# Performance work log

Measured on AMD Instinct MI355X. Metric: run time of the kernel, lower is better.

The kernel has to match this reference:

```python
import jax, jax.numpy as jnp
import numpy as np

EPS = 1e-6
NUM_HEADS = 16


def setup_inputs() -> dict:
    key = jax.random.key(0)
    ks = jax.random.split(key, 11)
    B, S, E = 2, 2048, 1024
    sc = 1.0 / np.sqrt(E)
    return {
        "x": jax.random.normal(ks[0], (B, S, E), dtype=jnp.float32),
        "Wq": jax.random.normal(ks[1], (E, E), dtype=jnp.float32) * sc,
        "bq": jax.random.normal(ks[2], (E,), dtype=jnp.float32) * 0.01,
        "Wk": jax.random.normal(ks[3], (E, E), dtype=jnp.float32) * sc,
        "bk": jax.random.normal(ks[4], (E,), dtype=jnp.float32) * 0.01,
        "Wv": jax.random.normal(ks[5], (E, E), dtype=jnp.float32) * sc,
        "bv": jax.random.normal(ks[6], (E,), dtype=jnp.float32) * 0.01,
        "Wp": jax.random.normal(ks[7], (E, E), dtype=jnp.float32) * sc,
        "bp": jax.random.normal(ks[8], (E,), dtype=jnp.float32) * 0.01,
        "gain": jax.random.uniform(ks[9], (E,), dtype=jnp.float32),
        "beta": jax.random.normal(ks[10], (E,), dtype=jnp.float32),
    }


def _layer_norm(x, gain, beta):
    # torch: (x - mean) / (std + eps) * gain + bias, std with Bessel correction
    mean = jnp.mean(x, axis=-1, keepdims=True)
    std = jnp.std(x, axis=-1, keepdims=True, ddof=1)
    return (x - mean) / (std + EPS) * gain + beta


def reference(x, Wq, bq, Wk, bk, Wv, bv, Wp, bp, gain, beta):
    B, S, E = x.shape
    H = NUM_HEADS
    D = E // H
    # QKV projections, split heads: [B,S,E] -> [B,H,S,D]
    def heads(y):
        return y.reshape(B, S, H, D).transpose(0, 2, 1, 3)
    q = heads(x @ Wq + bq)
    k = heads(x @ Wk + bk)
    v = heads(x @ Wv + bv)
    # scores [B,H,S,S], mask=None path (no causal mask applied in forward)
    scores = jnp.einsum("bhid,bhjd->bhij", q, k) / jnp.sqrt(jnp.float32(D))
    attn = jax.nn.softmax(scores, axis=-1)  # dropout is identity at eval
    y = jnp.einsum("bhij,bhjd->bhid", attn, v)
    y = y.transpose(0, 2, 1, 3).reshape(B, S, E)
    return _layer_norm(y @ Wp + bp, gain, beta)
```

## Files before the change

### kernel.cpp

```cpp
#include <hip/hip_runtime.h>
#include <hip/hip_bf16.h>
#include <math.h>

constexpr int Bc = 2;
constexpr int Sc = 2048;
constexpr int Ec = 1024;
constexpr int Hc = 16;
constexpr int Dc = 64;

typedef __attribute__((ext_vector_type(8))) short short8;
typedef __attribute__((ext_vector_type(4))) short short4v;
typedef __attribute__((ext_vector_type(4))) int int4v;
typedef __attribute__((ext_vector_type(4))) float f32x4;

__device__ inline unsigned short f2bf(float x) {
    __hip_bfloat16 h = __float2bfloat16(x);
    return *reinterpret_cast<unsigned short*>(&h);
}

__device__ inline f32x4 mfma16(short8 a, short8 b, f32x4 c) {
    return __builtin_amdgcn_mfma_f32_16x16x32_bf16(a, b, c, 0, 0, 0);
}

__device__ inline float exp2_fast(float x) {
    float r;
    asm("v_exp_f32 %0, %1" : "=v"(r) : "v"(x));
    return r;
}

__device__ inline int cvt_pk_bf16(float lo, float hi) {
    int r;
    asm("v_cvt_pk_bf16_f32 %0, %1, %2" : "=v"(r) : "v"(lo), "v"(hi));
    return r;
}

__device__ inline void gload_lds16(const unsigned short* gsrc, unsigned short* ldst) {
    __builtin_amdgcn_global_load_lds(
        (const __attribute__((address_space(1))) unsigned int*)(const void*)gsrc,
        (__attribute__((address_space(3))) unsigned int*)(void*)ldst,
        16, 0, 0);
}

__global__ __launch_bounds__(256) void prep_kernel(
    const float* __restrict__ X, unsigned short* __restrict__ Xb,
    const float* __restrict__ W0, const float* __restrict__ W1,
    const float* __restrict__ W2, const float* __restrict__ W3,
    unsigned short* __restrict__ T0, unsigned short* __restrict__ T1,
    unsigned short* __restrict__ T2, unsigned short* __restrict__ T3)
{
    __shared__ unsigned short Ls[64][72];
    const int bid = blockIdx.x, t = threadIdx.x;
    if (bid < 2048) {
        int i = bid * 256 + t;
        const float4* src = (const float4*)(X + (size_t)i * 8);
        float4 a = src[0], b = src[1];
        short8 o;
        o[0] = f2bf(a.x); o[1] = f2bf(a.y); o[2] = f2bf(a.z); o[3] = f2bf(a.w);
        o[4] = f2bf(b.x); o[5] = f2bf(b.y); o[6] = f2bf(b.z); o[7] = f2bf(b.w);
        *(short8*)(Xb + (size_t)i * 8) = o;
        return;
    }
    const int tt = bid - 2048;
    const float* W; unsigned short* T;
    switch (tt >> 8) {
        case 0: W = W0; T = T0; break;
        case 1: W = W1; T = T1; break;
        case 2: W = W2; T = T2; break;
        default: W = W3; T = T3; break;
    }
    const int rem = tt & 255;
    const int n0 = (rem & 15) * 64, k0 = (rem >> 4) * 64;
    {
        int k = t >> 2, nb = (t & 3) * 16;
        const float* src = W + (size_t)(k0 + k) * Ec + n0 + nb;
#pragma unroll
        for (int j = 0; j < 16; ++j) Ls[k][nb + j] = f2bf(src[j]);
    }
    __syncthreads();
    {
        int n = t >> 2, kb = (t & 3) * 16;
        short8 o0, o1;
#pragma unroll
        for (int j = 0; j < 8; ++j) { o0[j] = Ls[kb + j][n]; o1[j] = Ls[kb + 8 + j][n]; }
        unsigned short* dst = T + (size_t)(n0 + n) * Ec + k0 + kb;
        *(short8*)dst = o0;
        *(short8*)(dst + 8) = o1;
    }
}

constexpr int BM = 128, BK = 64;

template<int BNt>
__device__ __forceinline__ void gemm_core_t(
    const unsigned short* __restrict__ A, const unsigned short* __restrict__ Bt,
    const float* __restrict__ bias, float* __restrict__ Cf,
    unsigned short* __restrict__ Cb, int M, int N, int K, int mode, float oscale)
{
    constexpr int NW = BNt / 32;
    constexpr int WN = BNt / 2;
    constexpr int CH = (BM + BNt) / 8;
    constexpr int PW = CH / 4;
    __shared__ unsigned short lds[2][(BM + BNt) * BK];
    const int tid = threadIdx.x, lane = tid & 63, wid = tid >> 6;
    const int c16 = lane & 15, g = lane >> 4;
    const int wr = wid >> 1, wc = wid & 1;
    const int row0 = blockIdx.y * BM, col0 = blockIdx.x * BNt;

    const int rsub = lane >> 3;
    const int colE = ((lane & 7) ^ rsub) * 8;

    f32x4 acc[4][NW] = {};

    auto stage = [&](int buf, int k0) {
        unsigned short* Ab = &lds[buf][0];
        unsigned short* Bb = &lds[buf][BM * BK];
#pragma unroll
        for (int i = 0; i < PW; ++i) {
            int c = wid * PW + i;
            if (c < 16) {
                const unsigned short* src = A + (size_t)(row0 + c * 8 + rsub) * K + k0 + colE;
                gload_lds16(src, Ab + c * 512);
            } else {
                int c2 = c - 16;
                const unsigned short* src = Bt + (size_t)(col0 + c2 * 8 + rsub) * K + k0 + colE;
                gload_lds16(src, Bb + c2 * 512);
            }
        }
    };

    stage(0, 0);
    __syncthreads();
    int cur = 0;
    const int NT = K / BK;
    for (int t = 0; t < NT; ++t) {
        if (t + 1 < NT) stage(cur ^ 1, (t + 1) * BK);
        const unsigned short* Ab = &lds[cur][0];
        const unsigned short* Bb = &lds[cur][BM * BK];
#pragma unroll
        for (int kk = 0; kk < 2; ++kk) {
            const int cb = ((kk * 64 + g * 16) ^ ((c16 & 7) << 4)) >> 1;
            short8 af[4], bfr[NW];
#pragma unroll
            for (int m = 0; m < 4; ++m) {
                int row = wr * 64 + m * 16 + c16;
                af[m] = *(const short8*)(Ab + row * BK + cb);
            }
#pragma unroll
            for (int n = 0; n < NW; ++n) {
                int row = wc * WN + n * 16 + c16;
                bfr[n] = *(const short8*)(Bb + row * BK + cb);
            }
#pragma unroll
            for (int m = 0; m < 4; ++m)
#pragma unroll
                for (int n = 0; n < NW; ++n)
                    acc[m][n] = mfma16(af[m], bfr[n], acc[m][n]);
        }
        __syncthreads();
        cur ^= 1;
    }

#pragma unroll
    for (int m = 0; m < 4; ++m) {
#pragma unroll
        for (int n = 0; n < NW; ++n) {
            int gc = col0 + wc * WN + n * 16 + c16;
            float bi = bias[gc];
            if (mode == 2) {
                int h = gc >> 6, d = gc & (Dc - 1);
                int s0 = row0 + wr * 64 + m * 16 + g * 4;
                int a = (s0 >> 2) & 7;
                int sp = (s0 & ~31) + ((a & 3) << 3) + ((a >> 2) << 2);
                int b = s0 >> 11, s = sp & (Sc - 1);
                short4v pk;
#pragma unroll
                for (int r = 0; r < 4; ++r)
                    pk[r] = (short)f2bf((acc[m][n][r] + bi) * oscale);
                *(short4v*)&Cb[(((size_t)b * Hc + h) * Dc + d) * Sc + s] = pk;
            } else {
#pragma unroll
                for (int r = 0; r < 4; ++r) {
                    int gr = row0 + wr * 64 + m * 16 + g * 4 + r;
                    float v = (acc[m][n][r] + bi) * oscale;
                    if (mode == 0) {
                        Cf[(size_t)gr * N + gc] = v;
                    } else {
                        int b = gr >> 11, s = gr & (Sc - 1);
                        int h = gc >> 6, d = gc & (Dc - 1);
                        Cb[(((size_t)b * Hc + h) * Sc + s) * Dc + d] = f2bf(v);
                    }
                }
            }
        }
    }
}

__global__ __launch_bounds__(256) void gemm_mfma_kernel(
    const unsigned short* __restrict__ A, const unsigned short* __restrict__ Bt,
    const float* __restrict__ bias, float* __restrict__ Cf, int M, int N, int K)
{
    gemm_core_t<64>(A, Bt, bias, Cf, nullptr, M, N, K, 0, 1.0f);
}

__global__ __launch_bounds__(256) void qkv_gemm_kernel(
    const unsigned short* __restrict__ A,
    const unsigned short* __restrict__ WqT, const unsigned short* __restrict__ WkT,
    const unsigned short* __restrict__ WvT,
    const float* __restrict__ bq, const float* __restrict__ bk,
    const float* __restrict__ bv,
    unsigned short* __restrict__ Qb, unsigned short* __restrict__ Kb,
    unsigned short* __restrict__ Vt, int M, int N, int K, float sl2e)
{
    if (blockIdx.z == 0)      gemm_core_t<128>(A, WqT, bq, nullptr, Qb, M, N, K, 1, sl2e);
    else if (blockIdx.z == 1) gemm_core_t<128>(A, WkT, bk, nullptr, Kb, M, N, K, 1, 1.0f);
    else                      gemm_core_t<128>(A, WvT, bv, nullptr, Vt, M, N, K, 2, 1.0f);
}

__global__ __launch_bounds__(256) void attn_mfma_kernel(
    const unsigned short* __restrict__ Q, const unsigned short* __restrict__ K,
    const unsigned short* __restrict__ Vt, unsigned short* __restrict__ Y)
{
    __shared__ __align__(16) unsigned short lds[2][2][64 * 64];

    const int tid  = threadIdx.x;
    const int lane = tid & 63, wid = tid >> 6;
    const int g = lane >> 4, c16 = lane & 15;
    const int bh = blockIdx.x;
    const int qw = blockIdx.y * 128 + wid * 32;
    const size_t base = (size_t)bh * Sc * Dc;

    short8 bq[2][2];
#pragma unroll
    for (int u = 0; u < 2; ++u) {
        const unsigned short* Qp = Q + base + (size_t)(qw + u * 16 + c16) * Dc;
        bq[u][0] = *(const short8*)(Qp + g * 8);
        bq[u][1] = *(const short8*)(Qp + 32 + g * 8);
    }

    const int rsub = lane >> 3;
    const int srcoffE = 8 * ((lane & 7) ^ rsub);
    const int row0g = (wid * 2 + 0) * 8 + rsub;
    const int row1g = (wid * 2 + 1) * 8 + rsub;

    const unsigned short* kg0 = K  + base + (size_t)row0g * Dc + srcoffE;
    const unsigned short* kg1 = K  + base + (size_t)row1g * Dc + srcoffE;
    const unsigned short* vg0 = Vt + base + (size_t)row0g * Sc + srcoffE;
    const unsigned short* vg1 = Vt + base + (size_t)row1g * Sc + srcoffE;

    f32x4 o[2][4] = {};
    float psacc[2] = {0.f, 0.f};

    auto stage = [&](unsigned short* kbuf, unsigned short* vbuf) {
        gload_lds16(kg0, kbuf + (wid * 2 + 0) * 512);
        gload_lds16(kg1, kbuf + (wid * 2 + 1) * 512);
        gload_lds16(vg0, vbuf + (wid * 2 + 0) * 512);
        gload_lds16(vg1, vbuf + (wid * 2 + 1) * 512);
        kg0 += 64 * Dc; kg1 += 64 * Dc;
        vg0 += 64;      vg1 += 64;
    };

    const int sw = (c16 & 7) << 4;

    auto compute = [&](const unsigned short* kbuf, const unsigned short* vbuf) {
        const char* kbc = (const char*)kbuf;
        const char* vbc = (const char*)vbuf;

        f32x4 c[2][4];
        __builtin_amdgcn_s_setprio(1);
#pragma unroll
        for (int ct = 0; ct < 4; ++ct) {
            const int kr = ct * 16 + c16;
            short8 alo = *(const short8*)(kbc + kr * 128 + ((16 * g) ^ sw));
            short8 ahi = *(const short8*)(kbc + kr * 128 + ((64 + 16 * g) ^ sw));
            f32x4 z0 = {}, z1 = {};
            z0 = mfma16(alo, bq[0][0], z0);
            c[0][ct] = mfma16(ahi, bq[0][1], z0);
            z1 = mfma16(alo, bq[1][0], z1);
            c[1][ct] = mfma16(ahi, bq[1][1], z1);
        }
        __builtin_amdgcn_s_setprio(0);

        int4v p32[2][2];
#pragma unroll
        for (int u = 0; u < 2; ++u) {
            float ps = 0.f;
#pragma unroll
            for (int ct = 0; ct < 4; ++ct) {
                float p0 = exp2_fast(c[u][ct][0]);
                float p1 = exp2_fast(c[u][ct][1]);
                float p2 = exp2_fast(c[u][ct][2]);
                float p3 = exp2_fast(c[u][ct][3]);
                ps += (p0 + p1) + (p2 + p3);
                p32[u][ct >> 1][(ct & 1) * 2 + 0] = cvt_pk_bf16(p0, p1);
                p32[u][ct >> 1][(ct & 1) * 2 + 1] = cvt_pk_bf16(p2, p3);
            }
            psacc[u] += ps;
        }

        __builtin_amdgcn_s_setprio(1);
#pragma unroll
        for (int dt = 0; dt < 4; ++dt) {
            const int drow = dt * 16 + c16;
#pragma unroll
            for (int w = 0; w < 2; ++w) {
                short8 va = *(const short8*)(vbc + drow * 128 + ((w * 64 + 16 * g) ^ sw));
                o[0][dt] = mfma16(va, __builtin_bit_cast(short8, p32[0][w]), o[0][dt]);
                o[1][dt] = mfma16(va, __builtin_bit_cast(short8, p32[1][w]), o[1][dt]);
            }
        }
        __builtin_amdgcn_s_setprio(0);
    };

    unsigned short* k0b = &lds[0][0][0]; unsigned short* v0b = &lds[0][1][0];
    unsigned short* k1b = &lds[1][0][0]; unsigned short* v1b = &lds[1][1][0];

    constexpr int NT = Sc / 64;
    stage(k0b, v0b);
    for (int kt = 0; kt < NT; kt += 2) {
        asm volatile("s_waitcnt vmcnt(0)" ::: "memory");
        __builtin_amdgcn_s_barrier();
        __builtin_amdgcn_sched_barrier(0);
        if (kt + 1 < NT) stage(k1b, v1b);
        compute(k0b, v0b);
        asm volatile("s_waitcnt vmcnt(0)" ::: "memory");
        __builtin_amdgcn_s_barrier();
        __builtin_amdgcn_sched_barrier(0);
        if (kt + 2 < NT) stage(k0b, v0b);
        compute(k1b, v1b);
    }

    const int b = bh >> 4, h = bh & (Hc - 1);
#pragma unroll
    for (int u = 0; u < 2; ++u) {
        float ps = psacc[u];
        ps += __shfl_xor(ps, 16);
        ps += __shfl_xor(ps, 32);
        const float inv = 1.f / ps;
        const int qg = qw + u * 16 + c16;
        unsigned short* yrow = Y + ((size_t)b * Sc + qg) * Ec + h * Dc;
#pragma unroll
        for (int dt = 0; dt < 4; ++dt)
#pragma unroll
            for (int r = 0; r < 4; ++r)
                yrow[dt * 16 + g * 4 + r] = f2bf(o[u][dt][r] * inv);
    }
}

__global__ __launch_bounds__(256) void ln_kernel(
    const float* __restrict__ Z, const float* __restrict__ gain,
    const float* __restrict__ beta, float* __restrict__ out)
{
    __shared__ float red0[4];
    __shared__ float red1[4];
    const int row = blockIdx.x;
    const int t = threadIdx.x;
    const float4* z4 = (const float4*)(Z + (size_t)row * Ec);
    float4 v = z4[t];

    float s = v.x + v.y + v.z + v.w;
#pragma unroll
    for (int off = 32; off > 0; off >>= 1) s += __shfl_down(s, off);
    if ((t & 63) == 0) red0[t >> 6] = s;
    __syncthreads();
    float mean = (red0[0] + red0[1] + red0[2] + red0[3]) * (1.0f / Ec);

    float dx = v.x - mean; float vs = dx * dx;
    dx = v.y - mean; vs += dx * dx;
    dx = v.z - mean; vs += dx * dx;
    dx = v.w - mean; vs += dx * dx;
#pragma unroll
    for (int off = 32; off > 0; off >>= 1) vs += __shfl_down(vs, off);
    if ((t & 63) == 0) red1[t >> 6] = vs;
    __syncthreads();
    float var = (red1[0] + red1[1] + red1[2] + red1[3]) * (1.0f / (Ec - 1));
    float inv = 1.0f / (sqrtf(var) + 1e-6f);

    float4 g = ((const float4*)gain)[t];
    float4 bb = ((const float4*)beta)[t];
    float4 o;
    o.x = (v.x - mean) * inv * g.x + bb.x;
    o.y = (v.y - mean) * inv * g.y + bb.y;
    o.z = (v.z - mean) * inv * g.z + bb.z;
    o.w = (v.w - mean) * inv * g.w + bb.w;
    ((float4*)(out + (size_t)row * Ec))[t] = o;
}

extern "C" void kernel_launch(void* const* d_in, const int* in_sizes, int n_in,
                              void* d_out, int out_size, void* d_ws, size_t ws_size,
                              hipStream_t stream)
{
    const float* x    = (const float*)d_in[0];
    const float* Wq   = (const float*)d_in[1];
    const float* bq   = (const float*)d_in[2];
    const float* Wk   = (const float*)d_in[3];
    const float* bk   = (const float*)d_in[4];
    const float* Wv   = (const float*)d_in[5];
    const float* bv   = (const float*)d_in[6];
    const float* Wp   = (const float*)d_in[7];
    const float* bp   = (const float*)d_in[8];
    const float* gain = (const float*)d_in[9];
    const float* beta = (const float*)d_in[10];

    const int M = Bc * Sc;
    const size_t MK  = (size_t)M * Ec;
    const size_t EE  = (size_t)Ec * Ec;

    unsigned short* xb  = (unsigned short*)d_ws;
    unsigned short* wqt = xb + MK;
    unsigned short* wkt = wqt + EE;
    unsigned short* wvt = wkt + EE;
    unsigned short* wpt = wvt + EE;
    unsigned short* qb  = wpt + EE;
    unsigned short* kb  = qb + MK;
    unsigned short* vt  = kb + MK;
    unsigned short* yb  = vt + MK;

    float* z = (float*)qb;

    const float sl2e = 0.125f * 1.44269504f;

    prep_kernel<<<3072, 256, 0, stream>>>(x, xb, Wq, Wk, Wv, Wp, wqt, wkt, wvt, wpt);

    dim3 qkv_grid(Ec / 128, M / BM, 3);
    qkv_gemm_kernel<<<qkv_grid, 256, 0, stream>>>(
        xb, wqt, wkt, wvt, bq, bk, bv, qb, kb, vt, M, Ec, Ec, sl2e);

    dim3 attn_grid(Bc * Hc, Sc / 128);
    attn_mfma_kernel<<<attn_grid, 256, 0, stream>>>(qb, kb, vt, yb);

    dim3 proj_grid(Ec / 64, M / BM);
    gemm_mfma_kernel<<<proj_grid, 256, 0, stream>>>(yb, wpt, bp, z, M, Ec, Ec);

    ln_kernel<<<M, 256, 0, stream>>>(z, gain, beta, (float*)d_out);
}
```

Before: 118.6 us.

## Compute softmax row sums via MFMA, store projection output as bf16

The attention kernel drops the per-lane scalar accumulation of exp values and the cross-lane shuffles. Instead it gets softmax denominators from an extra MFMA that multiplies a ones matrix by the P tile, and it packs the output stores into vectorized bf16 writes. The output projection now writes its pre-LayerNorm result as bf16 instead of fp32, which halves the bytes written and then read by the LayerNorm kernel. The cost is bf16 rounding of values before normalization, which adds error, plus the denominator being summed from bf16-rounded probabilities.

After: 116.1 us (median of 2 runs). -2.1%, faster.

```diff
diff --git a/kernel.cpp b/kernel.cpp
--- a/kernel.cpp
+++ b/kernel.cpp
@@ -10,12 +10,18 @@
 
 typedef __attribute__((ext_vector_type(8))) short short8;
 typedef __attribute__((ext_vector_type(4))) short short4v;
+typedef __attribute__((ext_vector_type(2))) int int2v;
 typedef __attribute__((ext_vector_type(4))) int int4v;
 typedef __attribute__((ext_vector_type(4))) float f32x4;
 
 __device__ inline unsigned short f2bf(float x) {
     __hip_bfloat16 h = __float2bfloat16(x);
     return *reinterpret_cast<unsigned short*>(&h);
+}
+
+__device__ inline float bf2f(unsigned short u) {
+    unsigned int v = (unsigned int)u << 16;
+    return __builtin_bit_cast(float, v);
 }
 
 __device__ inline f32x4 mfma16(short8 a, short8 b, f32x4 c) {
@@ -184,6 +190,8 @@
                     float v = (acc[m][n][r] + bi) * oscale;
                     if (mode == 0) {
                         Cf[(size_t)gr * N + gc] = v;
+                    } else if (mode == 3) {
+                        Cb[(size_t)gr * N + gc] = f2bf(v);
                     } else {
                         int b = gr >> 11, s = gr & (Sc - 1);
                         int h = gc >> 6, d = gc & (Dc - 1);
@@ -197,9 +205,10 @@
 
 __global__ __launch_bounds__(256) void gemm_mfma_kernel(
     const unsigned short* __restrict__ A, const unsigned short* __restrict__ Bt,
-    const float* __restrict__ bias, float* __restrict__ Cf, int M, int N, int K)
-{
-    gemm_core_t<64>(A, Bt, bias, Cf, nullptr, M, N, K, 0, 1.0f);
+    const float* __restrict__ bias, unsigned short* __restrict__ Cb,
+    int M, int N, int K)
+{
+    gemm_core_t<64>(A, Bt, bias, nullptr, Cb, M, N, K, 3, 1.0f);
 }
 
 __global__ __launch_bounds__(256) void qkv_gemm_kernel(
@@ -248,7 +257,9 @@
     const unsigned short* vg1 = Vt + base + (size_t)row1g * Sc + srcoffE;
 
     f32x4 o[2][4] = {};
-    float psacc[2] = {0.f, 0.f};
+    f32x4 acc_ps[2] = {};
+    const short8 ones8 = {(short)0x3F80, (short)0x3F80, (short)0x3F80, (short)0x3F80,
+                          (short)0x3F80, (short)0x3F80, (short)0x3F80, (short)0x3F80};
 
     auto stage = [&](unsigned short* kbuf, unsigned short* vbuf) {
         gload_lds16(kg0, kbuf + (wid * 2 + 0) * 512);
@@ -283,29 +294,30 @@
         int4v p32[2][2];
 #pragma unroll
         for (int u = 0; u < 2; ++u) {
-            float ps = 0.f;
 #pragma unroll
             for (int ct = 0; ct < 4; ++ct) {
                 float p0 = exp2_fast(c[u][ct][0]);
                 float p1 = exp2_fast(c[u][ct][1]);
                 float p2 = exp2_fast(c[u][ct][2]);
                 float p3 = exp2_fast(c[u][ct][3]);
-                ps += (p0 + p1) + (p2 + p3);
                 p32[u][ct >> 1][(ct & 1) * 2 + 0] = cvt_pk_bf16(p0, p1);
                 p32[u][ct >> 1][(ct & 1) * 2 + 1] = cvt_pk_bf16(p2, p3);
             }
-            psacc[u] += ps;
         }
 
         __builtin_amdgcn_s_setprio(1);
 #pragma unroll
-        for (int dt = 0; dt < 4; ++dt) {
-            const int drow = dt * 16 + c16;
-#pragma unroll
-            for (int w = 0; w < 2; ++w) {
+        for (int w = 0; w < 2; ++w) {
+            short8 pb0 = __builtin_bit_cast(short8, p32[0][w]);
+            short8 pb1 = __builtin_bit_cast(short8, p32[1][w]);
+            acc_ps[0] = mfma16(ones8, pb0, acc_ps[0]);
+            acc_ps[1] = mfma16(ones8, pb1, acc_ps[1]);
+#pragma unroll
+            for (int dt = 0; dt < 4; ++dt) {
+                const int drow = dt * 16 + c16;
                 short8 va = *(const short8*)(vbc + drow * 128 + ((w * 64 + 16 * g) ^ sw));
-                o[0][dt] = mfma16(va, __builtin_bit_cast(short8, p32[0][w]), o[0][dt]);
-                o[1][dt] = mfma16(va, __builtin_bit_cast(short8, p32[1][w]), o[1][dt]);
+                o[0][dt] = mfma16(va, pb0, o[0][dt]);
+                o[1][dt] = mfma16(va, pb1, o[1][dt]);
             }
         }
         __builtin_amdgcn_s_setprio(0);
@@ -332,42 +344,44 @@
     const int b = bh >> 4, h = bh & (Hc - 1);
 #pragma unroll
     for (int u = 0; u < 2; ++u) {
-        float ps = psacc[u];
-        ps += __shfl_xor(ps, 16);
-        ps += __shfl_xor(ps, 32);
-        const float inv = 1.f / ps;
+        const float inv = 1.f / acc_ps[u][0];
         const int qg = qw + u * 16 + c16;
         unsigned short* yrow = Y + ((size_t)b * Sc + qg) * Ec + h * Dc;
 #pragma unroll
-        for (int dt = 0; dt < 4; ++dt)
-#pragma unroll
-            for (int r = 0; r < 4; ++r)
-                yrow[dt * 16 + g * 4 + r] = f2bf(o[u][dt][r] * inv);
+        for (int dt = 0; dt < 4; ++dt) {
+            int2v wv;
+            wv[0] = cvt_pk_bf16(o[u][dt][0] * inv, o[u][dt][1] * inv);
+            wv[1] = cvt_pk_bf16(o[u][dt][2] * inv, o[u][dt][3] * inv);
+            *(int2v*)&yrow[dt * 16 + g * 4] = wv;
+        }
     }
 }
 
 __global__ __launch_bounds__(256) void ln_kernel(
-    const float* __restrict__ Z, const float* __restrict__ gain,
+    const unsigned short* __restrict__ Z, const float* __restrict__ gain,
     const float* __restrict__ beta, float* __restrict__ out)
 {
     __shared__ float red0[4];
     __shared__ float red1[4];
     const int row = blockIdx.x;
     const int t = threadIdx.x;
-    const float4* z4 = (const float4*)(Z + (size_t)row * Ec);
-    float4 v = z4[t];
-
-    float s = v.x + v.y + v.z + v.w;
+    short4v zv = *(const short4v*)(Z + (size_t)row * Ec + t * 4);
+    float v0 = bf2f((unsigned short)zv[0]);
+    float v1 = bf2f((unsigned short)zv[1]);
+    float v2 = bf2f((unsigned short)zv[2]);
+    float v3 = bf2f((unsigned short)zv[3]);
+
+    float s = (v0 + v1) + (v2 + v3);
 #pragma unroll
     for (int off = 32; off > 0; off >>= 1) s += __shfl_down(s, off);
     if ((t & 63) == 0) red0[t >> 6] = s;
     __syncthreads();
     float mean = (red0[0] + red0[1] + red0[2] + red0[3]) * (1.0f / Ec);
 
-    float dx = v.x - mean; float vs = dx * dx;
-    dx = v.y - mean; vs += dx * dx;
-    dx = v.z - mean; vs += dx * dx;
-    dx = v.w - mean; vs += dx * dx;
+    float dx = v0 - mean; float vs = dx * dx;
+    dx = v1 - mean; vs += dx * dx;
+    dx = v2 - mean; vs += dx * dx;
+    dx = v3 - mean; vs += dx * dx;
 #pragma unroll
     for (int off = 32; off > 0; off >>= 1) vs += __shfl_down(vs, off);
     if ((t & 63) == 0) red1[t >> 6] = vs;
@@ -375,13 +389,13 @@
     float var = (red1[0] + red1[1] + red1[2] + red1[3]) * (1.0f / (Ec - 1));
     float inv = 1.0f / (sqrtf(var) + 1e-6f);
 
-    float4 g = ((const float4*)gain)[t];
+    float4 gn = ((const float4*)gain)[t];
     float4 bb = ((const float4*)beta)[t];
     float4 o;
-    o.x = (v.x - mean) * inv * g.x + bb.x;
-    o.y = (v.y - mean) * inv * g.y + bb.y;
-    o.z = (v.z - mean) * inv * g.z + bb.z;
-    o.w = (v.w - mean) * inv * g.w + bb.w;
+    o.x = (v0 - mean) * inv * gn.x + bb.x;
+    o.y = (v1 - mean) * inv * gn.y + bb.y;
+    o.z = (v2 - mean) * inv * gn.z + bb.z;
+    o.w = (v3 - mean) * inv * gn.w + bb.w;
     ((float4*)(out + (size_t)row * Ec))[t] = o;
 }
 
@@ -415,7 +429,7 @@
     unsigned short* vt  = kb + MK;
     unsigned short* yb  = vt + MK;
 
-    float* z = (float*)qb;
+    unsigned short* zb = qb;
 
     const float sl2e = 0.125f * 1.44269504f;
 
@@ -429,7 +443,7 @@
     attn_mfma_kernel<<<attn_grid, 256, 0, stream>>>(qb, kb, vt, yb);
 
     dim3 proj_grid(Ec / 64, M / BM);
-    gemm_mfma_kernel<<<proj_grid, 256, 0, stream>>>(yb, wpt, bp, z, M, Ec, Ec);
-
-    ln_kernel<<<M, 256, 0, stream>>>(z, gain, beta, (float*)d_out);
-}
+    gemm_mfma_kernel<<<proj_grid, 256, 0, stream>>>(yb, wpt, bp, zb, M, Ec, Ec);
+
+    ln_kernel<<<M, 256, 0, stream>>>(zb, gain, beta, (float*)d_out);
+}
```
